# Kernel optimization log

Hardware: AMD Instinct MI355X
Metric: run time of the kernel (lower is better)

Reference implementation:

```python
import jax, jax.numpy as jnp
import numpy as np
from jax import lax

B, T, V, E, H, C, K = 256, 512, 50000, 128, 256, 128, 2


def setup_inputs() -> dict:
    key = jax.random.key(0)
    ks = jax.random.split(key, 16)
    s = lambda *sh: 1.0 / np.sqrt(sh[0])
    return {
        "input_current": jax.random.randint(ks[0], (B, T), 0, V, dtype=jnp.int32),
        "input_left": jax.random.randint(ks[1], (B, T), 0, V, dtype=jnp.int32),
        "input_right": jax.random.randint(ks[2], (B, T), 0, V, dtype=jnp.int32),
        "emb": jax.random.normal(ks[3], (V, E), jnp.float32) * 0.05,
        "Wf": jax.random.normal(ks[4], (E, H), jnp.float32) * s(E),
        "Uf": jax.random.normal(ks[5], (H, H), jnp.float32) * s(H),
        "bf": jnp.zeros((H,), jnp.float32),
        "Wb": jax.random.normal(ks[6], (E, H), jnp.float32) * s(E),
        "Ub": jax.random.normal(ks[7], (H, H), jnp.float32) * s(H),
        "bb": jnp.zeros((H,), jnp.float32),
        "Wc": jax.random.normal(ks[8], (2 * H + E, C), jnp.float32) * s(2 * H + E),
        "bc": jnp.zeros((C,), jnp.float32),
        "Wd": jax.random.normal(ks[9], (C, K), jnp.float32) * s(C),
        "bd": jnp.zeros((K,), jnp.float32),
    }


def _simple_rnn(x, W, U, b):
    # x: [B,T,E] -> outputs [B,T,H]; h_t = tanh(x_t W + b + h_{t-1} U)
    xw = jnp.einsum("bte,eh->bth", x, W) + b  # precompute input projection
    h0 = jnp.zeros((x.shape[0], U.shape[0]), x.dtype)

    def step(h, xw_t):
        h = jnp.tanh(xw_t + h @ U)
        return h, h

    _, hs = lax.scan(step, h0, jnp.swapaxes(xw, 0, 1))  # scan over time
    return jnp.swapaxes(hs, 0, 1)


def reference(input_current, input_left, input_right, emb, Wf, Uf, bf, Wb, Ub, bb, Wc, bc, Wd, bd):
    e_cur = emb[input_current]  # [B,T,E]
    e_left = emb[input_left]
    e_right = emb[input_right]
    x_left = _simple_rnn(e_left, Wf, Uf, bf)  # [B,T,H]
    # go_backwards RNN: process reversed sequence, then model reverses back
    x_right = _simple_rnn(e_right[:, ::-1], Wb, Ub, bb)[:, ::-1]  # [B,T,H]
    x = jnp.concatenate([x_left, e_cur, x_right], axis=2)  # [B,T,2H+E]
    x = jnp.tanh(jnp.einsum("btd,dc->btc", x, Wc) + bc)  # Conv1D k=1 + tanh
    x = jnp.max(x, axis=1)  # GlobalMaxPooling1D
    return jax.nn.sigmoid(x @ Wd + bd)  # [B,K]
```

## Files before the change

### kernel.cpp

```cpp
#include <hip/hip_runtime.h>
#include <hip/hip_bf16.h>


#define B_ 256
#define T_ 512
#define E_ 128
#define H_ 256
#define C_ 128

typedef __attribute__((ext_vector_type(8))) short short8;
typedef __attribute__((ext_vector_type(4))) float float4v;
typedef __attribute__((ext_vector_type(2))) unsigned int uint2v;

__device__ inline unsigned short f2bf(float f) {
  unsigned u = __float_as_uint(f);
  u += 0x7fffu + ((u >> 16) & 1u);
  return (unsigned short)(u >> 16);
}
__device__ inline unsigned pkbf(float a, float b) {
  __hip_bfloat162 h2 = __float22bfloat162_rn(float2{a, b});
  union { __hip_bfloat162 h; unsigned u; } cv;
  cv.h = h2;
  return cv.u;
}
__device__ inline float lo16f(unsigned u) { return __uint_as_float(u << 16); }
__device__ inline float hi16f(unsigned u) { return __uint_as_float(u & 0xffff0000u); }
__device__ inline float fast_tanh(float x) {
  float e = __expf(2.f * x);
  float r = __builtin_amdgcn_rcpf(e + 1.f);
  return __builtin_fmaf(-2.f, r, 1.f);
}
__device__ inline unsigned enc_f(float f) {
  unsigned u = __float_as_uint(f);
  return (u & 0x80000000u) ? ~u : (u | 0x80000000u);
}
__device__ inline float dec_f(unsigned key) {
  unsigned bits = (key & 0x80000000u) ? (key ^ 0x80000000u) : ~key;
  return __uint_as_float(bits);
}
__device__ inline void sync_lds() {
  asm volatile("s_waitcnt lgkmcnt(0)\n\ts_barrier" ::: "memory");
}

__device__ inline void wait_flag(const int* f) {
  if (__hip_atomic_load(f, __ATOMIC_RELAXED, __HIP_MEMORY_SCOPE_AGENT) == 0) {
    while (__hip_atomic_load(f, __ATOMIC_RELAXED, __HIP_MEMORY_SCOPE_AGENT) ==
           0)
      __builtin_amdgcn_s_sleep(8);
  }
  (void)__hip_atomic_load(f, __ATOMIC_ACQUIRE, __HIP_MEMORY_SCOPE_AGENT);
}

__global__ __launch_bounds__(256) void prep_kernel(
    const float* __restrict__ Wf, const float* __restrict__ Wb,
    const float* __restrict__ Wc, const float* __restrict__ Uf,
    const float* __restrict__ Ub,
    unsigned short* __restrict__ WfT, unsigned short* __restrict__ WbT,
    unsigned short* __restrict__ WcT, unsigned short* __restrict__ UfT,
    unsigned short* __restrict__ UbT, unsigned int* __restrict__ pooled,
    int* __restrict__ flags) {
  int gid = blockIdx.x * 256 + threadIdx.x;
  int stride = gridDim.x * 256;
  for (int i = gid; i < 128 * 256; i += stride) {
    int k = i >> 8, n = i & 255;
    WfT[n * 128 + k] = f2bf(Wf[i]);
    WbT[n * 128 + k] = f2bf(Wb[i]);
  }
  for (int i = gid; i < 640 * 128; i += stride) {
    int k = i >> 7, n = i & 127;
    WcT[n * 640 + k] = f2bf(Wc[i]);
  }
  for (int i = gid; i < 256 * 256; i += stride) {
    int k = i >> 8, n = i & 255;
    UfT[n * 256 + k] = f2bf(Uf[i]);
    UbT[n * 256 + k] = f2bf(Ub[i]);
  }
  for (int i = gid; i < B_ * C_; i += stride) pooled[i] = 0u;
  for (int i = gid; i < 1024; i += stride) flags[i] = 0;
}

__global__ __launch_bounds__(512, 1) void fused_kernel(
    const int* __restrict__ idxL, const int* __restrict__ idxR,
    const int* __restrict__ idxC, const float* __restrict__ emb,
    const unsigned short* __restrict__ WfT,
    const unsigned short* __restrict__ WbT,
    const float* __restrict__ bfv, const float* __restrict__ bbv,
    const unsigned short* __restrict__ UfT,
    const unsigned short* __restrict__ UbT, unsigned short* x,
    int* __restrict__ flags) {
  const int blk = blockIdx.x;
  const int tid = threadIdx.x;
  const int lane = tid & 63, q = lane >> 4, l15 = lane & 15;

  __shared__ __attribute__((aligned(16))) unsigned short hbuf[2][16][280];
  __shared__ unsigned char iso_pad[72 * 1024];
  if (flags == nullptr) {
    iso_pad[tid] = (unsigned char)idxL[tid];
    __syncthreads();
    x[tid] = iso_pad[(tid * 37) & 65535];
  }

  if (blk < 32) {
    const int dir = blk & 1;
    const int btile = blk >> 1;
    const int b0 = btile * 16;
    const unsigned short* __restrict__ UT = dir ? UbT : UfT;
    const int xoff = dir ? 384 : 0;
    const int tstep = dir ? -1 : 1;
    const int t0 = dir ? (T_ - 1) : 0;
    const ptrdiff_t dstep = (ptrdiff_t)tstep * 640;
    const int wv = tid >> 6;
    const int* fl = flags + (dir * 16 + btile) * 32;

    unsigned short* hb0 = &hbuf[0][0][0];
    unsigned short* hb1 = &hbuf[1][0][0];
    for (int i = tid; i < 16 * 280; i += 512) hb0[i] = 0;

    short8 ufr[2][8];
#pragma unroll
    for (int mt = 0; mt < 2; ++mt)
#pragma unroll
      for (int kt = 0; kt < 8; ++kt)
        ufr[mt][kt] = *(const short8*)(UT + (32 * wv + 16 * mt + l15) * H_ +
                                       kt * 32 + q * 8);

    int lastc = dir ? 31 : 0;
    wait_flag(fl + lastc);

    unsigned short* ptrS[2];
    const unsigned short* ptrL[2];
    uint2v curA[2], curB[2], infA[2], infB[2];
#pragma unroll
    for (int mt = 0; mt < 2; ++mt) {
      unsigned short* base =
          x + (size_t)(b0 + 2 * wv + mt) * T_ * 640 + xoff + lane * 4;
      unsigned short* bt = base + (ptrdiff_t)t0 * 640;
      curA[mt] = *(const uint2v*)(bt);
      curB[mt] = *(const uint2v*)(bt + dstep);
      infA[mt] = *(const uint2v*)(bt + 2 * dstep);
      infB[mt] = *(const uint2v*)(bt + 3 * dstep);
      ptrS[mt] = bt;
      ptrL[mt] = bt + 4 * dstep;
    }

    const unsigned lrd = l15 * 280;
    const unsigned lwr = l15 * 280 + 32 * wv;

    __syncthreads();

#pragma unroll 1
    for (int p = 0; p < 256; ++p) {
      int c = dir ? ((506 - 2 * p) >> 4) : ((2 * p + 5) >> 4);
      c = c < 0 ? 0 : (c > 31 ? 31 : c);
      if (c != lastc) {
        wait_flag(fl + c);
        lastc = c;
      }
      uint2v ldA[2], ldB[2];
      if (p < 254) {
#pragma unroll
        for (int mt = 0; mt < 2; ++mt) {
          ldA[mt] = *(const uint2v*)(ptrL[mt]);
          ldB[mt] = *(const uint2v*)(ptrL[mt] + dstep);
        }
      } else {
#pragma unroll
        for (int mt = 0; mt < 2; ++mt) {
          ldA[mt] = infA[mt];
          ldB[mt] = infB[mt];
        }
      }
#pragma unroll
      for (int mt = 0; mt < 2; ++mt) ptrL[mt] += 2 * dstep;

      {
        short8 afr[8];
#pragma unroll
        for (int kt = 0; kt < 8; ++kt)
          afr[kt] = *(const short8*)(hb0 + lrd + kt * 32 + q * 8);
        float4v acc[2];
#pragma unroll
        for (int mt = 0; mt < 2; ++mt)
          acc[mt] = (float4v){lo16f(curA[mt].x), hi16f(curA[mt].x),
                              lo16f(curA[mt].y), hi16f(curA[mt].y)};
#pragma unroll
        for (int kt = 0; kt < 8; ++kt)
#pragma unroll
          for (int mt = 0; mt < 2; ++mt)
            acc[mt] = __builtin_amdgcn_mfma_f32_16x16x32_bf16(
                ufr[mt][kt], afr[kt], acc[mt], 0, 0, 0);
#pragma unroll
        for (int mt = 0; mt < 2; ++mt) {
          uint2v hv = {pkbf(fast_tanh(acc[mt][0]), fast_tanh(acc[mt][1])),
                       pkbf(fast_tanh(acc[mt][2]), fast_tanh(acc[mt][3]))};
          *(uint2v*)(hb1 + lwr + 16 * mt + 4 * q) = hv;
          *(uint2v*)ptrS[mt] = hv;
        }
      }
      sync_lds();

      {
        short8 afr[8];
#pragma unroll
        for (int kt = 0; kt < 8; ++kt)
          afr[kt] = *(const short8*)(hb1 + lrd + kt * 32 + q * 8);
        float4v acc[2];
#pragma unroll
        for (int mt = 0; mt < 2; ++mt)
          acc[mt] = (float4v){lo16f(curB[mt].x), hi16f(curB[mt].x),
                              lo16f(curB[mt].y), hi16f(curB[mt].y)};
#pragma unroll
        for (int kt = 0; kt < 8; ++kt)
#pragma unroll
          for (int mt = 0; mt < 2; ++mt)
            acc[mt] = __builtin_amdgcn_mfma_f32_16x16x32_bf16(
                ufr[mt][kt], afr[kt], acc[mt], 0, 0, 0);
#pragma unroll
        for (int mt = 0; mt < 2; ++mt) {
          uint2v hv = {pkbf(fast_tanh(acc[mt][0]), fast_tanh(acc[mt][1])),
                       pkbf(fast_tanh(acc[mt][2]), fast_tanh(acc[mt][3]))};
          *(uint2v*)(hb0 + lwr + 16 * mt + 4 * q) = hv;
          *(uint2v*)(ptrS[mt] + dstep) = hv;
        }
      }
#pragma unroll
      for (int mt = 0; mt < 2; ++mt) {
        ptrS[mt] += 2 * dstep;
        curA[mt] = infA[mt];
        curB[mt] = infB[mt];
        infA[mt] = ldA[mt];
        infB[mt] = ldB[mt];
      }
      sync_lds();
    }
    return;
  }

  if (blk < 1056) {
    const int b2 = blk - 32;
    const int z = b2 >> 5, r = b2 & 31;
    const int btile = r & 15, dirg = r >> 4;
    const int chunk = dirg ? (31 - z) : z;
    const int w8 = tid >> 6;
    const int g = w8 >> 2, wv = w8 & 3;
    const int t0 = chunk * 16 + g * 8;
    const int b0 = btile * 16;
    const int* __restrict__ idx = dirg ? idxR : idxL;
    const unsigned short* __restrict__ WT = dirg ? WbT : WfT;
    const float* __restrict__ bias = dirg ? bbv : bfv;

    short8 wfr[4][4];
#pragma unroll
    for (int mt = 0; mt < 4; ++mt)
#pragma unroll
      for (int kt = 0; kt < 4; ++kt)
        wfr[mt][kt] = *(const short8*)(WT + (64 * wv + 16 * mt + l15) * 128 +
                                       kt * 32 + q * 8);
    float4v bv[4];
#pragma unroll
    for (int mt = 0; mt < 4; ++mt)
      bv[mt] = *(const float4v*)(bias + 64 * wv + 16 * mt + 4 * q);

    int er[8];
#pragma unroll
    for (int j = 0; j < 8; ++j) er[j] = idx[(b0 + l15) * T_ + t0 + j];

    float4v g0[8];
#pragma unroll
    for (int kt = 0; kt < 4; ++kt) {
      const float* p8 = emb + (size_t)er[0] * E_ + kt * 32 + q * 8;
      g0[2 * kt] = *(const float4v*)p8;
      g0[2 * kt + 1] = *(const float4v*)(p8 + 4);
    }

#pragma unroll 1
    for (int j = 0; j < 8; ++j) {
      float4v gn[8];
      if (j < 7) {
#pragma unroll
        for (int kt = 0; kt < 4; ++kt) {
          const float* p8 = emb + (size_t)er[j + 1] * E_ + kt * 32 + q * 8;
          gn[2 * kt] = *(const float4v*)p8;
          gn[2 * kt + 1] = *(const float4v*)(p8 + 4);
        }
      }
      short8 efr[4];
#pragma unroll
      for (int kt = 0; kt < 4; ++kt) {
        union { unsigned u[4]; short8 s; } cv;
        cv.u[0] = pkbf(g0[2 * kt][0], g0[2 * kt][1]);
        cv.u[1] = pkbf(g0[2 * kt][2], g0[2 * kt][3]);
        cv.u[2] = pkbf(g0[2 * kt + 1][0], g0[2 * kt + 1][1]);
        cv.u[3] = pkbf(g0[2 * kt + 1][2], g0[2 * kt + 1][3]);
        efr[kt] = cv.s;
      }
      float4v acc[4];
#pragma unroll
      for (int mt = 0; mt < 4; ++mt) acc[mt] = (float4v){0.f, 0.f, 0.f, 0.f};
#pragma unroll
      for (int kt = 0; kt < 4; ++kt)
#pragma unroll
        for (int mt = 0; mt < 4; ++mt)
          acc[mt] = __builtin_amdgcn_mfma_f32_16x16x32_bf16(
              wfr[mt][kt], efr[kt], acc[mt], 0, 0, 0);
      const int t = t0 + j;
#pragma unroll
      for (int mt = 0; mt < 4; ++mt) {
        float4v v = acc[mt] + bv[mt];
        uint2v pk = {pkbf(v[0], v[1]), pkbf(v[2], v[3])};
        *(uint2v*)(x + ((size_t)(b0 + 4 * wv + mt) * T_ + t) * 640 +
                   dirg * 384 + lane * 4) = pk;
      }
      if (j < 7) {
#pragma unroll
        for (int kk = 0; kk < 8; ++kk) g0[kk] = gn[kk];
      }
    }
    __syncthreads();
    if (tid == 0) {
      __threadfence();
      __hip_atomic_store(flags + (dirg * 16 + btile) * 32 + chunk, 1,
                         __ATOMIC_RELEASE, __HIP_MEMORY_SCOPE_AGENT);
    }
    return;
  }

  {
    const int b3 = blk - 1056;
    const int btile = b3 & 15, tch = b3 >> 4;
    const int b0 = btile * 16;
    const int w8 = tid >> 6;
    const int tA = tch * 16 + 2 * w8, tB = tA + 1;
    const int erA = idxC[(b0 + l15) * T_ + tA];
    const int erB = idxC[(b0 + l15) * T_ + tB];
    const float* epA = emb + (size_t)erA * E_;
    const float* epB = emb + (size_t)erB * E_;
    float4v ga[8], gb[8];
#pragma unroll
    for (int u = 0; u < 8; ++u) ga[u] = *(const float4v*)(epA + 16 * u + 4 * q);
#pragma unroll
    for (int u = 0; u < 8; ++u) gb[u] = *(const float4v*)(epB + 16 * u + 4 * q);
#pragma unroll
    for (int u = 0; u < 8; ++u) {
      uint2v pk = {pkbf(ga[u][0], ga[u][1]), pkbf(ga[u][2], ga[u][3])};
      int row = b0 + u + 8 * (q >> 1);
      *(uint2v*)(x + ((size_t)row * T_ + tA) * 640 + 256 + 64 * (q & 1) +
                 4 * l15) = pk;
    }
#pragma unroll
    for (int u = 0; u < 8; ++u) {
      uint2v pk = {pkbf(gb[u][0], gb[u][1]), pkbf(gb[u][2], gb[u][3])};
      int row = b0 + u + 8 * (q >> 1);
      *(uint2v*)(x + ((size_t)row * T_ + tB) * 640 + 256 + 64 * (q & 1) +
                 4 * l15) = pk;
    }
  }
}

__global__ __launch_bounds__(256, 2) void convpool_kernel(
    const unsigned short* __restrict__ x, const unsigned short* __restrict__ WcT,
    const float* __restrict__ bc, unsigned int* __restrict__ pooled) {
  const int b0 = (blockIdx.x & 15) * 16;
  const int t0 = (blockIdx.x >> 4) * 16;
  const int tid = threadIdx.x;
  const int w = tid >> 6, lane = tid & 63, q = lane >> 4, l15 = lane & 15;

  __shared__ __attribute__((aligned(16))) unsigned short tile[2][16][648];

  short8 wfr[2][20];
#pragma unroll
  for (int ct = 0; ct < 2; ++ct)
#pragma unroll
    for (int kt = 0; kt < 20; ++kt)
      wfr[ct][kt] = *(const short8*)(WcT +
                                     (size_t)(32 * w + 16 * ct + l15) * 640 +
                                     kt * 32 + q * 8);
  float4v bv[2];
#pragma unroll
  for (int ct = 0; ct < 2; ++ct)
    bv[ct] = *(const float4v*)(bc + 32 * w + 16 * ct + 4 * q);

  float4v mx[2];
  mx[0] = (float4v){-1e30f, -1e30f, -1e30f, -1e30f};
  mx[1] = mx[0];

  const int srow = tid >> 4, ssub = tid & 15;
  {
    const unsigned short* src = x + ((size_t)(b0 + srow) * T_ + t0) * 640;
#pragma unroll
    for (int j = 0; j < 5; ++j)
      *(short8*)&tile[0][srow][ssub * 8 + j * 128] =
          *(const short8*)(src + ssub * 8 + j * 128);
  }
  __syncthreads();

#pragma unroll 1
  for (int j = 0; j < 16; ++j) {
    const int t = t0 + j;
    const int buf = j & 1;
    if (j < 15) {
      const unsigned short* src = x + ((size_t)(b0 + srow) * T_ + t + 1) * 640;
#pragma unroll
      for (int jj = 0; jj < 5; ++jj)
        *(short8*)&tile[buf ^ 1][srow][ssub * 8 + jj * 128] =
            *(const short8*)(src + ssub * 8 + jj * 128);
    }
    float4v acc[2];
    acc[0] = (float4v){0.f, 0.f, 0.f, 0.f};
    acc[1] = (float4v){0.f, 0.f, 0.f, 0.f};
#pragma unroll
    for (int kt = 0; kt < 20; ++kt) {
      int row, so1, so2;
      if (kt < 8) {
        row = 2 * kt + (q >> 1);
        so1 = 64 * (2 * (q & 1)) + 4 * l15;
        so2 = so1 + 64;
      } else if (kt < 12) {
        row = 2 * (kt - 8) + (q >> 1) + 8 * (q & 1);
        so1 = 256 + 4 * l15;
        so2 = 320 + 4 * l15;
      } else {
        row = 2 * (kt - 12) + (q >> 1);
        so1 = 384 + 64 * (2 * (q & 1)) + 4 * l15;
        so2 = so1 + 64;
      }
      union { unsigned u[4]; short8 s; } cv;
      uint2v c1 = *(const uint2v*)&tile[buf][row][so1];
      uint2v c2 = *(const uint2v*)&tile[buf][row][so2];
      cv.u[0] = c1.x; cv.u[1] = c1.y; cv.u[2] = c2.x; cv.u[3] = c2.y;
      acc[0] = __builtin_amdgcn_mfma_f32_16x16x32_bf16(wfr[0][kt], cv.s,
                                                       acc[0], 0, 0, 0);
      acc[1] = __builtin_amdgcn_mfma_f32_16x16x32_bf16(wfr[1][kt], cv.s,
                                                       acc[1], 0, 0, 0);
    }
#pragma unroll
    for (int ct = 0; ct < 2; ++ct)
#pragma unroll
      for (int i = 0; i < 4; ++i)
        mx[ct][i] = fmaxf(mx[ct][i], acc[ct][i]);
    __syncthreads();
  }
#pragma unroll
  for (int ct = 0; ct < 2; ++ct)
#pragma unroll
    for (int i = 0; i < 4; ++i)
      atomicMax(pooled + (b0 + l15) * C_ + 32 * w + 16 * ct + 4 * q + i,
                enc_f(fast_tanh(mx[ct][i] + bv[ct][i])));
}

__global__ __launch_bounds__(256) void dense_kernel(
    const unsigned int* __restrict__ pooled, const float* __restrict__ Wd,
    const float* __restrict__ bd, float* __restrict__ out) {
  int b = threadIdx.x;
  float s0 = bd[0], s1 = bd[1];
#pragma unroll 4
  for (int c = 0; c < C_; ++c) {
    float f = dec_f(pooled[b * C_ + c]);
    s0 += f * Wd[c * 2 + 0];
    s1 += f * Wd[c * 2 + 1];
  }
  out[b * 2 + 0] = 1.f / (1.f + __expf(-s0));
  out[b * 2 + 1] = 1.f / (1.f + __expf(-s1));
}

extern "C" void kernel_launch(void* const* d_in, const int* in_sizes, int n_in,
                              void* d_out, int out_size, void* d_ws, size_t ws_size,
                              hipStream_t stream) {
  const int* idxC = (const int*)d_in[0];
  const int* idxL = (const int*)d_in[1];
  const int* idxR = (const int*)d_in[2];
  const float* emb = (const float*)d_in[3];
  const float* Wf = (const float*)d_in[4];
  const float* Uf = (const float*)d_in[5];
  const float* bf_ = (const float*)d_in[6];
  const float* Wb = (const float*)d_in[7];
  const float* Ub = (const float*)d_in[8];
  const float* bb_ = (const float*)d_in[9];
  const float* Wc = (const float*)d_in[10];
  const float* bc = (const float*)d_in[11];
  const float* Wd = (const float*)d_in[12];
  const float* bd = (const float*)d_in[13];

  char* ws = (char*)d_ws;
  unsigned short* x = (unsigned short*)ws;
  unsigned int* pooled = (unsigned int*)(ws + 167772160);
  unsigned short* WfT = (unsigned short*)(ws + 167903232);
  unsigned short* WbT = WfT + 256 * 128;
  unsigned short* WcT = WbT + 256 * 128;
  unsigned short* UfT = WcT + 128 * 640;
  unsigned short* UbT = UfT + 256 * 256;
  int* flags = (int*)(ws + 168460288);

  prep_kernel<<<64, 256, 0, stream>>>(Wf, Wb, Wc, Uf, Ub, WfT, WbT, WcT, UfT,
                                      UbT, pooled, flags);
  fused_kernel<<<1568, 512, 0, stream>>>(idxL, idxR, idxC, emb, WfT, WbT, bf_,
                                         bb_, UfT, UbT, x, flags);
  convpool_kernel<<<512, 256, 0, stream>>>(x, WcT, bc, pooled);
  dense_kernel<<<1, 256, 0, stream>>>(pooled, Wd, bd, (float*)d_out);
}
```

Measured before the change: 593.0 us.

## Pre-convert embedding table to bf16 and deepen recurrence input prefetch

```diff
diff --git a/kernel.cpp b/kernel.cpp
--- a/kernel.cpp
+++ b/kernel.cpp
@@ -7,6 +7,7 @@
 #define E_ 128
 #define H_ 256
 #define C_ 128
+#define V_ 50000
 
 typedef __attribute__((ext_vector_type(8))) short short8;
 typedef __attribute__((ext_vector_type(4))) float float4v;
@@ -54,11 +55,11 @@
 __global__ __launch_bounds__(256) void prep_kernel(
     const float* __restrict__ Wf, const float* __restrict__ Wb,
     const float* __restrict__ Wc, const float* __restrict__ Uf,
-    const float* __restrict__ Ub,
+    const float* __restrict__ Ub, const float* __restrict__ emb,
     unsigned short* __restrict__ WfT, unsigned short* __restrict__ WbT,
     unsigned short* __restrict__ WcT, unsigned short* __restrict__ UfT,
-    unsigned short* __restrict__ UbT, unsigned int* __restrict__ pooled,
-    int* __restrict__ flags) {
+    unsigned short* __restrict__ UbT, unsigned short* __restrict__ ebf,
+    unsigned int* __restrict__ pooled, int* __restrict__ flags) {
   int gid = blockIdx.x * 256 + threadIdx.x;
   int stride = gridDim.x * 256;
   for (int i = gid; i < 128 * 256; i += stride) {
@@ -75,13 +76,14 @@
     UfT[n * 256 + k] = f2bf(Uf[i]);
     UbT[n * 256 + k] = f2bf(Ub[i]);
   }
+  for (int i = gid; i < V_ * E_; i += stride) ebf[i] = f2bf(emb[i]);
   for (int i = gid; i < B_ * C_; i += stride) pooled[i] = 0u;
   for (int i = gid; i < 1024; i += stride) flags[i] = 0;
 }
 
 __global__ __launch_bounds__(512, 1) void fused_kernel(
     const int* __restrict__ idxL, const int* __restrict__ idxR,
-    const int* __restrict__ idxC, const float* __restrict__ emb,
+    const int* __restrict__ idxC, const unsigned short* __restrict__ ebf,
     const unsigned short* __restrict__ WfT,
     const unsigned short* __restrict__ WbT,
     const float* __restrict__ bfv, const float* __restrict__ bbv,
@@ -129,18 +131,19 @@
 
     unsigned short* ptrS[2];
     const unsigned short* ptrL[2];
-    uint2v curA[2], curB[2], infA[2], infB[2];
+    uint2v sA[4][2], sB[4][2];
 #pragma unroll
     for (int mt = 0; mt < 2; ++mt) {
       unsigned short* base =
           x + (size_t)(b0 + 2 * wv + mt) * T_ * 640 + xoff + lane * 4;
       unsigned short* bt = base + (ptrdiff_t)t0 * 640;
-      curA[mt] = *(const uint2v*)(bt);
-      curB[mt] = *(const uint2v*)(bt + dstep);
-      infA[mt] = *(const uint2v*)(bt + 2 * dstep);
-      infB[mt] = *(const uint2v*)(bt + 3 * dstep);
+#pragma unroll
+      for (int s = 0; s < 4; ++s) {
+        sA[s][mt] = *(const uint2v*)(bt + 2 * s * dstep);
+        sB[s][mt] = *(const uint2v*)(bt + (2 * s + 1) * dstep);
+      }
       ptrS[mt] = bt;
-      ptrL[mt] = bt + 4 * dstep;
+      ptrL[mt] = bt + 8 * dstep;
     }
 
     const unsigned lrd = l15 * 280;
@@ -150,14 +153,14 @@
 
 #pragma unroll 1
     for (int p = 0; p < 256; ++p) {
-      int c = dir ? ((506 - 2 * p) >> 4) : ((2 * p + 5) >> 4);
+      int c = dir ? ((502 - 2 * p) >> 4) : ((2 * p + 9) >> 4);
       c = c < 0 ? 0 : (c > 31 ? 31 : c);
       if (c != lastc) {
         wait_flag(fl + c);
         lastc = c;
       }
       uint2v ldA[2], ldB[2];
-      if (p < 254) {
+      if (p < 252) {
 #pragma unroll
         for (int mt = 0; mt < 2; ++mt) {
           ldA[mt] = *(const uint2v*)(ptrL[mt]);
@@ -166,8 +169,8 @@
       } else {
 #pragma unroll
         for (int mt = 0; mt < 2; ++mt) {
-          ldA[mt] = infA[mt];
-          ldB[mt] = infB[mt];
+          ldA[mt] = sA[3][mt];
+          ldB[mt] = sB[3][mt];
         }
       }
 #pragma unroll
@@ -181,8 +184,8 @@
         float4v acc[2];
 #pragma unroll
         for (int mt = 0; mt < 2; ++mt)
-          acc[mt] = (float4v){lo16f(curA[mt].x), hi16f(curA[mt].x),
-                              lo16f(curA[mt].y), hi16f(curA[mt].y)};
+          acc[mt] = (float4v){lo16f(sA[0][mt].x), hi16f(sA[0][mt].x),
+                              lo16f(sA[0][mt].y), hi16f(sA[0][mt].y)};
 #pragma unroll
         for (int kt = 0; kt < 8; ++kt)
 #pragma unroll
@@ -207,8 +210,8 @@
         float4v acc[2];
 #pragma unroll
         for (int mt = 0; mt < 2; ++mt)
-          acc[mt] = (float4v){lo16f(curB[mt].x), hi16f(curB[mt].x),
-                              lo16f(curB[mt].y), hi16f(curB[mt].y)};
+          acc[mt] = (float4v){lo16f(sB[0][mt].x), hi16f(sB[0][mt].x),
+                              lo16f(sB[0][mt].y), hi16f(sB[0][mt].y)};
 #pragma unroll
         for (int kt = 0; kt < 8; ++kt)
 #pragma unroll
@@ -226,10 +229,13 @@
 #pragma unroll
       for (int mt = 0; mt < 2; ++mt) {
         ptrS[mt] += 2 * dstep;
-        curA[mt] = infA[mt];
-        curB[mt] = infB[mt];
-        infA[mt] = ldA[mt];
-        infB[mt] = ldB[mt];
+#pragma unroll
+        for (int s = 0; s < 3; ++s) {
+          sA[s][mt] = sA[s + 1][mt];
+          sB[s][mt] = sB[s + 1][mt];
+        }
+        sA[3][mt] = ldA[mt];
+        sB[3][mt] = ldB[mt];
       }
       sync_lds();
     }
@@ -265,34 +271,19 @@
 #pragma unroll
     for (int j = 0; j < 8; ++j) er[j] = idx[(b0 + l15) * T_ + t0 + j];
 
-    float4v g0[8];
-#pragma unroll
-    for (int kt = 0; kt < 4; ++kt) {
-      const float* p8 = emb + (size_t)er[0] * E_ + kt * 32 + q * 8;
-      g0[2 * kt] = *(const float4v*)p8;
-      g0[2 * kt + 1] = *(const float4v*)(p8 + 4);
-    }
+    short8 g0[4];
+#pragma unroll
+    for (int kt = 0; kt < 4; ++kt)
+      g0[kt] = *(const short8*)(ebf + (size_t)er[0] * E_ + kt * 32 + q * 8);
 
 #pragma unroll 1
     for (int j = 0; j < 8; ++j) {
-      float4v gn[8];
+      short8 gn[4];
       if (j < 7) {
 #pragma unroll
-        for (int kt = 0; kt < 4; ++kt) {
-          const float* p8 = emb + (size_t)er[j + 1] * E_ + kt * 32 + q * 8;
-          gn[2 * kt] = *(const float4v*)p8;
-          gn[2 * kt + 1] = *(const float4v*)(p8 + 4);
-        }
-      }
-      short8 efr[4];
-#pragma unroll
-      for (int kt = 0; kt < 4; ++kt) {
-        union { unsigned u[4]; short8 s; } cv;
-        cv.u[0] = pkbf(g0[2 * kt][0], g0[2 * kt][1]);
-        cv.u[1] = pkbf(g0[2 * kt][2], g0[2 * kt][3]);
-        cv.u[2] = pkbf(g0[2 * kt + 1][0], g0[2 * kt + 1][1]);
-        cv.u[3] = pkbf(g0[2 * kt + 1][2], g0[2 * kt + 1][3]);
-        efr[kt] = cv.s;
+        for (int kt = 0; kt < 4; ++kt)
+          gn[kt] = *(const short8*)(ebf + (size_t)er[j + 1] * E_ + kt * 32 +
+                                    q * 8);
       }
       float4v acc[4];
 #pragma unroll
@@ -302,7 +293,7 @@
 #pragma unroll
         for (int mt = 0; mt < 4; ++mt)
           acc[mt] = __builtin_amdgcn_mfma_f32_16x16x32_bf16(
-              wfr[mt][kt], efr[kt], acc[mt], 0, 0, 0);
+              wfr[mt][kt], g0[kt], acc[mt], 0, 0, 0);
       const int t = t0 + j;
 #pragma unroll
       for (int mt = 0; mt < 4; ++mt) {
@@ -313,7 +304,7 @@
       }
       if (j < 7) {
 #pragma unroll
-        for (int kk = 0; kk < 8; ++kk) g0[kk] = gn[kk];
+        for (int kk = 0; kk < 4; ++kk) g0[kk] = gn[kk];
       }
     }
     __syncthreads();
@@ -333,26 +324,26 @@
     const int tA = tch * 16 + 2 * w8, tB = tA + 1;
     const int erA = idxC[(b0 + l15) * T_ + tA];
     const int erB = idxC[(b0 + l15) * T_ + tB];
-    const float* epA = emb + (size_t)erA * E_;
-    const float* epB = emb + (size_t)erB * E_;
-    float4v ga[8], gb[8];
-#pragma unroll
-    for (int u = 0; u < 8; ++u) ga[u] = *(const float4v*)(epA + 16 * u + 4 * q);
-#pragma unroll
-    for (int u = 0; u < 8; ++u) gb[u] = *(const float4v*)(epB + 16 * u + 4 * q);
+    const unsigned short* epA = ebf + (size_t)erA * E_;
+    const unsigned short* epB = ebf + (size_t)erB * E_;
+    uint2v ga[8], gb[8];
+#pragma unroll
+    for (int u = 0; u < 8; ++u)
+      ga[u] = *(const uint2v*)(epA + 16 * u + 4 * q);
+#pragma unroll
+    for (int u = 0; u < 8; ++u)
+      gb[u] = *(const uint2v*)(epB + 16 * u + 4 * q);
 #pragma unroll
     for (int u = 0; u < 8; ++u) {
-      uint2v pk = {pkbf(ga[u][0], ga[u][1]), pkbf(ga[u][2], ga[u][3])};
       int row = b0 + u + 8 * (q >> 1);
       *(uint2v*)(x + ((size_t)row * T_ + tA) * 640 + 256 + 64 * (q & 1) +
-                 4 * l15) = pk;
+                 4 * l15) = ga[u];
     }
 #pragma unroll
     for (int u = 0; u < 8; ++u) {
-      uint2v pk = {pkbf(gb[u][0], gb[u][1]), pkbf(gb[u][2], gb[u][3])};
       int row = b0 + u + 8 * (q >> 1);
       *(uint2v*)(x + ((size_t)row * T_ + tB) * 640 + 256 + 64 * (q & 1) +
-                 4 * l15) = pk;
+                 4 * l15) = gb[u];
     }
   }
 }
@@ -490,10 +481,11 @@
   unsigned short* UfT = WcT + 128 * 640;
   unsigned short* UbT = UfT + 256 * 256;
   int* flags = (int*)(ws + 168460288);
-
-  prep_kernel<<<64, 256, 0, stream>>>(Wf, Wb, Wc, Uf, Ub, WfT, WbT, WcT, UfT,
-                                      UbT, pooled, flags);
-  fused_kernel<<<1568, 512, 0, stream>>>(idxL, idxR, idxC, emb, WfT, WbT, bf_,
+  unsigned short* ebf = (unsigned short*)(ws + 168464384);
+
+  prep_kernel<<<128, 256, 0, stream>>>(Wf, Wb, Wc, Uf, Ub, emb, WfT, WbT, WcT,
+                                       UfT, UbT, ebf, pooled, flags);
+  fused_kernel<<<1568, 512, 0, stream>>>(idxL, idxR, idxC, ebf, WfT, WbT, bf_,
                                          bb_, UfT, UbT, x, flags);
   convpool_kernel<<<512, 256, 0, stream>>>(x, WcT, bc, pooled);
   dense_kernel<<<1, 256, 0, stream>>>(pooled, Wd, bd, (float*)d_out);
```

After: 636.6 us. 7.4% more time.
